# Performance work log

Measured on AMD Instinct MI355X. Metric: run time of the kernel, lower is better.

Reference implementation:

```python
import jax, jax.numpy as jnp
import numpy as np

EPS = 1e-06
BANDWIDTH = 0.1  # scipy minimize x0; frozen on first forward in the original


def _pairwise_sqdist(a, b):
    # a: [B, N, 3], b: [B, M, 3] -> [B, N, M] squared euclidean distances
    a2 = jnp.sum(a * a, axis=-1)  # [B, N]
    b2 = jnp.sum(b * b, axis=-1)  # [B, M]
    ab = jnp.einsum('bnd,bmd->bnm', a, b)  # [B, N, M]
    return jnp.maximum(a2[:, :, None] + b2[:, None, :] - 2.0 * ab, 0.0)


def _compute_density(points, bandwidth):
    # Gaussian KDE over all pairs (self included), normalized by N-1,
    # matching compute_density in the torch source.
    n = points.shape[1]
    sqd = _pairwise_sqdist(points, points)  # [B, N, N]
    kde = jnp.exp(-0.5 * sqd / (bandwidth * bandwidth))
    return jnp.sum(kde, axis=2) / (n - 1)  # [B, N]


def setup_inputs() -> dict:
    key = jax.random.key(0)
    k1, k2 = jax.random.split(key)
    predicted = jax.random.normal(k1, (8, 4096, 3), dtype=jnp.float32)
    ground_truth = jax.random.normal(k2, (8, 4096, 3), dtype=jnp.float32)
    return {
        'predicted': predicted,
        'ground_truth': ground_truth,
        'bandwidth_pred': jnp.float32(BANDWIDTH),
        'bandwidth_gt': jnp.float32(BANDWIDTH),
    }


def reference(predicted, ground_truth, bandwidth_pred, bandwidth_gt):
    # Chamfer distance: per-point squared distance to nearest neighbor in the
    # other cloud (standard ChamferDistance CUDA ext returns squared dists).
    sqd = _pairwise_sqdist(predicted, ground_truth)  # [B, N, M]
    dist_pred_to_gt = jnp.min(sqd, axis=2)  # [B, N]
    dist_gt_to_pred = jnp.min(sqd, axis=1)  # [B, M]

    density_pred = _compute_density(predicted, bandwidth_pred)  # [B, N]
    density_gt = _compute_density(ground_truth, bandwidth_gt)   # [B, M]

    loss_pred_to_gt = jnp.mean(dist_pred_to_gt / (density_pred + EPS))
    loss_gt_to_pred = jnp.mean(dist_gt_to_pred / (density_gt + EPS))
    return loss_pred_to_gt + loss_gt_to_pred
```

## Files before the change

kernel.cpp:

```cpp
#include <hip/hip_runtime.h>


#define NPTS 4096
#define NB   8
#define TS   128
#define TPB  256
#define BIGF 3.4e38f

__device__ __forceinline__ void unpack8(const float4* s4, int base,
                                        float (&X)[8], float (&Y)[8], float (&Z)[8])
{
    float4 A = s4[base+0], B = s4[base+1], C = s4[base+2];
    float4 D = s4[base+3], E = s4[base+4], F = s4[base+5];
    X[0]=A.x; Y[0]=A.y; Z[0]=A.z;  X[1]=A.w; Y[1]=B.x; Z[1]=B.y;
    X[2]=B.z; Y[2]=B.w; Z[2]=C.x;  X[3]=C.y; Y[3]=C.z; Z[3]=C.w;
    X[4]=D.x; Y[4]=D.y; Z[4]=D.z;  X[5]=D.w; Y[5]=E.x; Z[5]=E.y;
    X[6]=E.z; Y[6]=E.w; Z[6]=F.x;  X[7]=F.y; Y[7]=F.z; Z[7]=F.w;
}

__global__ __launch_bounds__(TPB) void dacl_pairs(
    const float* __restrict__ pred, const float* __restrict__ gt,
    const float* __restrict__ bwp,  const float* __restrict__ bwg,
    float* __restrict__ minP2G, float* __restrict__ minG2P,
    float* __restrict__ densP,  float* __restrict__ densG)
{
    __shared__ float4 sCol[1536];
    __shared__ float4 sRow[96];
    float* sRed = (float*)sCol;

    const int tid  = threadIdx.x;
    const int ty   = tid & 15;
    const int tx   = tid >> 4;
    const int wave = tid >> 6;
    const int lane = tid & 63;

    const int bid  = blockIdx.x;
    const int kind = bid % 6;
    const int rem  = bid / 6;
    const int b    = rem & 7;
    const int RT   = rem >> 3;

    const float* rowsrc; const float* colsrc; float scale;
    if (kind == 0)      { rowsrc = pred; colsrc = gt;   scale = 1.0f; }
    else if (kind == 1) { rowsrc = gt;   colsrc = pred; scale = 1.0f; }
    else if (kind < 4)  { rowsrc = pred; colsrc = pred;
                          const float bw = bwp[0];
                          scale = sqrtf(0.5f/(bw*bw*0.6931471805599453f)); }
    else                { rowsrc = gt;   colsrc = gt;
                          const float bw = bwg[0];
                          scale = sqrtf(0.5f/(bw*bw*0.6931471805599453f)); }

    const float4* rbase = (const float4*)(rowsrc + ((size_t)b*NPTS + RT*TS)*3);
    const float4* cbase = (const float4*)(colsrc + (size_t)b*NPTS*3);

    if (tid < 96) {
        float4 v = rbase[tid];
        v.x *= scale; v.y *= scale; v.z *= scale; v.w *= scale;
        sRow[tid] = v;
    }

    if (kind < 2) {
        float rx[8], ry[8], rz[8], rr[8], rmin[8];
        #pragma unroll
        for (int r = 0; r < 8; ++r) rmin[r] = BIGF;
        bool gotRows = false;

        for (int ph = 0; ph < 2; ++ph) {
            const float4* src = cbase + ph*1536;
            __syncthreads();
            #pragma unroll
            for (int i = 0; i < 6; ++i) sCol[tid + i*TPB] = src[tid + i*TPB];
            __syncthreads();
            if (!gotRows) {
                unpack8(sRow, ty*6, rx, ry, rz);
                #pragma unroll
                for (int r = 0; r < 8; ++r)
                    rr[r] = fmaf(rx[r],rx[r], fmaf(ry[r],ry[r], rz[r]*rz[r]));
                gotRows = true;
            }
            for (int t = 0; t < 16; ++t) {
                float cx[8], cy[8], cz[8];
                unpack8(sCol, t*96 + tx*6, cx, cy, cz);
                #pragma unroll
                for (int c = 0; c < 8; ++c) {
                    const float ax = -2.0f*cx[c], ay = -2.0f*cy[c], az = -2.0f*cz[c];
                    const float cc = fmaf(cx[c],cx[c], fmaf(cy[c],cy[c], cz[c]*cz[c]));
                    #pragma unroll
                    for (int r = 0; r < 8; ++r) {
                        float tv = fmaf(ax, rx[r], cc);
                        tv = fmaf(ay, ry[r], tv);
                        tv = fmaf(az, rz[r], tv);
                        rmin[r] = fminf(rmin[r], tv);
                    }
                }
            }
        }
        float v[8];
        #pragma unroll
        for (int r = 0; r < 8; ++r) {
            float m = fmaxf(rmin[r] + rr[r], 0.0f);
            m = fminf(m, __shfl_xor(m, 16, 64));
            m = fminf(m, __shfl_xor(m, 32, 64));
            v[r] = m;
        }
        __syncthreads();
        if (wave > 0 && lane < 16) {
            #pragma unroll
            for (int r = 0; r < 8; ++r) sRed[(wave-1)*128 + lane*8 + r] = v[r];
        }
        __syncthreads();
        if (wave == 0 && lane < 16) {
            float* out = (kind == 0 ? minP2G : minG2P) + b*NPTS + RT*TS + lane*8;
            #pragma unroll
            for (int r = 0; r < 8; ++r) {
                const int o = lane*8 + r;
                out[r] = fminf(fminf(v[r], sRed[o]),
                               fminf(sRed[128 + o], sRed[256 + o]));
            }
        }
    } else {
        const int h = kind & 1;
        float* D = (kind < 4 ? densP : densG) + h*(NB*NPTS);

        const float4* src = cbase + h*1536;
        #pragma unroll
        for (int i = 0; i < 6; ++i) {
            float4 x = src[tid + i*TPB];
            x.x *= scale; x.y *= scale; x.z *= scale; x.w *= scale;
            sCol[tid + i*TPB] = x;
        }
        __syncthreads();

        float rx[8], ry[8], rz[8], nrr[8], racc[8];
        unpack8(sRow, ty*6, rx, ry, rz);
        #pragma unroll
        for (int r = 0; r < 8; ++r) {
            nrr[r]  = -fmaf(rx[r],rx[r], fmaf(ry[r],ry[r], rz[r]*rz[r]));
            racc[r] = 0.0f;
        }

        for (int t = 0; t < 16; ++t) {
            float cx[8], cy[8], cz[8];
            unpack8(sCol, t*96 + tx*6, cx, cy, cz);
            #pragma unroll
            for (int c = 0; c < 8; ++c) {
                const float ax = 2.0f*cx[c], ay = 2.0f*cy[c], az = 2.0f*cz[c];
                const float ncc = fmaf(-cx[c],cx[c], fmaf(-cy[c],cy[c], -cz[c]*cz[c]));
                #pragma unroll
                for (int r = 0; r < 8; ++r) {
                    float e = fmaf(ax, rx[r], ncc);
                    e = fmaf(ay, ry[r], e);
                    e = fmaf(az, rz[r], e);
                    e = e + nrr[r];
                    racc[r] += __builtin_amdgcn_exp2f(e);
                }
            }
        }
        float v[8];
        #pragma unroll
        for (int r = 0; r < 8; ++r) {
            float s = racc[r];
            s += __shfl_xor(s, 16, 64);
            s += __shfl_xor(s, 32, 64);
            v[r] = s;
        }
        __syncthreads();
        if (wave > 0 && lane < 16) {
            #pragma unroll
            for (int r = 0; r < 8; ++r) sRed[(wave-1)*128 + lane*8 + r] = v[r];
        }
        __syncthreads();
        if (wave == 0 && lane < 16) {
            float* out = D + b*NPTS + RT*TS + lane*8;
            #pragma unroll
            for (int r = 0; r < 8; ++r) {
                const int o = lane*8 + r;
                out[r] = (v[r] + sRed[o]) + (sRed[128 + o] + sRed[256 + o]);
            }
        }
    }
}

__global__ __launch_bounds__(256) void dacl_combine(
    const float* __restrict__ minP2G, const float* __restrict__ minG2P,
    const float* __restrict__ densP, const float* __restrict__ densG,
    float* __restrict__ bsum)
{
    const int g   = blockIdx.x * 256 + threadIdx.x;
    const int dir = g >> 15;
    const int idx = g & 32767;
    const float m  = dir ? minG2P[idx] : minP2G[idx];
    const float dn = dir ? (densG[idx] + densG[idx + NB*NPTS])
                         : (densP[idx] + densP[idx + NB*NPTS]);
    float val = m / (dn * (1.0f/4095.0f) + 1e-6f) * (1.0f/32768.0f);

    #pragma unroll
    for (int off = 32; off; off >>= 1) val += __shfl_down(val, off);
    __shared__ float sm[4];
    const int lane = threadIdx.x & 63, wid = threadIdx.x >> 6;
    if (lane == 0) sm[wid] = val;
    __syncthreads();
    if (threadIdx.x == 0) bsum[blockIdx.x] = (sm[0] + sm[1]) + (sm[2] + sm[3]);
}

__global__ __launch_bounds__(256) void dacl_final(
    const float* __restrict__ bsum, float* __restrict__ out)
{
    float v = bsum[threadIdx.x];
    #pragma unroll
    for (int off = 32; off; off >>= 1) v += __shfl_down(v, off);
    __shared__ float sm[4];
    const int lane = threadIdx.x & 63, wid = threadIdx.x >> 6;
    if (lane == 0) sm[wid] = v;
    __syncthreads();
    if (threadIdx.x == 0) out[0] = (sm[0] + sm[1]) + (sm[2] + sm[3]);
}

extern "C" void kernel_launch(void* const* d_in, const int* in_sizes, int n_in,
                              void* d_out, int out_size, void* d_ws, size_t ws_size,
                              hipStream_t stream)
{
    const float* pred = (const float*)d_in[0];
    const float* gt   = (const float*)d_in[1];
    const float* bwp  = (const float*)d_in[2];
    const float* bwg  = (const float*)d_in[3];

    float* minP2G = (float*)d_ws;
    float* minG2P = minP2G + NB*NPTS;
    float* densP  = minG2P + NB*NPTS;
    float* densG  = densP + 2*NB*NPTS;
    float* bsum   = densG + 2*NB*NPTS;

    dacl_pairs<<<1536, TPB, 0, stream>>>(pred, gt, bwp, bwg,
                                         minP2G, minG2P, densP, densG);
    dacl_combine<<<(2*NB*NPTS)/256, 256, 0, stream>>>(minP2G, minG2P, densP, densG, bsum);
    dacl_final<<<1, 256, 0, stream>>>(bsum, (float*)d_out);
}
```

Before: 81.68 us.

## Compute pairwise dot products with bf16x3 split MFMA and exploit density symmetry

Adds a prep kernel that splits scaled coordinates into three bf16 parts and packs them into MFMA operand layouts. The pair kernel then computes the cross-term dot products with 16x16x32 bf16 MFMA instead of scalar FMAs. For the KDE it evaluates only the upper triangle of the symmetric kernel matrix and writes row and column partial sums separately. Chamfer minima are computed in both directions from one pass over the cross matrix. The goal is to move the inner products onto matrix cores and halve the exp work, at the cost of extra workspace traffic, a heavier combine step and some precision risk from the bf16 split.

Measured after the change: 127.0 us. 55.5% more time.

```diff
diff --git a/kernel.cpp b/kernel.cpp
--- a/kernel.cpp
+++ b/kernel.cpp
@@ -1,197 +1,296 @@
 #include <hip/hip_runtime.h>
 
 
+#define NB 8
 #define NPTS 4096
-#define NB   8
-#define TS   128
-#define TPB  256
+#define PTSTOT 32768
 #define BIGF 3.4e38f
-
-__device__ __forceinline__ void unpack8(const float4* s4, int base,
-                                        float (&X)[8], float (&Y)[8], float (&Z)[8])
-{
-    float4 A = s4[base+0], B = s4[base+1], C = s4[base+2];
-    float4 D = s4[base+3], E = s4[base+4], F = s4[base+5];
-    X[0]=A.x; Y[0]=A.y; Z[0]=A.z;  X[1]=A.w; Y[1]=B.x; Z[1]=B.y;
-    X[2]=B.z; Y[2]=B.w; Z[2]=C.x;  X[3]=C.y; Y[3]=C.z; Z[3]=C.w;
-    X[4]=D.x; Y[4]=D.y; Z[4]=D.z;  X[5]=D.w; Y[5]=E.x; Z[5]=E.y;
-    X[6]=E.z; Y[6]=E.w; Z[6]=F.x;  X[7]=F.y; Y[7]=F.z; Z[7]=F.w;
-}
-
-__global__ __launch_bounds__(TPB) void dacl_pairs(
+#define OFFD_BLKS 2176
+#define CROSS_BLKS 1024
+#define DIAG_BLKS 512
+#define TRISLOT 3968
+
+typedef __attribute__((ext_vector_type(8))) short bf16x8;
+typedef __attribute__((ext_vector_type(4))) float f32x4;
+
+__device__ __forceinline__ unsigned bf16rne(float x){
+    unsigned u = __float_as_uint(x);
+    return (u + 0x7FFFu + ((u>>16)&1u)) >> 16;
+}
+__device__ __forceinline__ void split1(float x, unsigned& h, unsigned& m, unsigned& l){
+    h = bf16rne(x);
+    float r1 = x - __uint_as_float(h<<16);
+    m = bf16rne(r1);
+    l = bf16rne(r1 - __uint_as_float(m<<16));
+}
+__device__ __forceinline__ void packA(uint4* a, int base,
+    unsigned hx,unsigned mx,unsigned lx, unsigned hy,unsigned my,unsigned ly,
+    unsigned hz,unsigned mz,unsigned lz)
+{
+    a[base]    = make_uint4(hx|(hx<<16), mx|(mx<<16), hx|(lx<<16), hy|(hy<<16));
+    a[base+16] = make_uint4(my|(my<<16), hy|(ly<<16), hz|(hz<<16), mz|(mz<<16));
+    a[base+32] = make_uint4(hz|(lz<<16), 0u, 0u, 0u);
+    a[base+48] = make_uint4(0u,0u,0u,0u);
+}
+__device__ __forceinline__ void packB(uint4* a, int base,
+    unsigned hx,unsigned mx,unsigned lx, unsigned hy,unsigned my,unsigned ly,
+    unsigned hz,unsigned mz,unsigned lz)
+{
+    a[base]    = make_uint4(hx|(mx<<16), hx|(mx<<16), lx|(hx<<16), hy|(my<<16));
+    a[base+16] = make_uint4(hy|(my<<16), ly|(hy<<16), hz|(mz<<16), hz|(mz<<16));
+    a[base+32] = make_uint4(lz|(hz<<16), 0u, 0u, 0u);
+    a[base+48] = make_uint4(0u,0u,0u,0u);
+}
+
+__global__ __launch_bounds__(256) void dacl_prep(
     const float* __restrict__ pred, const float* __restrict__ gt,
     const float* __restrict__ bwp,  const float* __restrict__ bwg,
-    float* __restrict__ minP2G, float* __restrict__ minG2P,
-    float* __restrict__ densP,  float* __restrict__ densG)
-{
-    __shared__ float4 sCol[1536];
-    __shared__ float4 sRow[96];
-    float* sRed = (float*)sCol;
-
+    uint4* __restrict__ Ac, uint4* __restrict__ Bc,
+    uint4* __restrict__ Ap, uint4* __restrict__ Bp,
+    uint4* __restrict__ Ag, uint4* __restrict__ Bg,
+    float* __restrict__ rrP, float* __restrict__ ccG,
+    float* __restrict__ ndP, float* __restrict__ ndG)
+{
+    const int gid  = blockIdx.x*256 + threadIdx.x;
+    const int cl   = gid >> 15;
+    const int pidx = gid & 32767;
+    const int base = ((pidx>>4)<<6) + (pidx & 15);
+    const float* s = (cl ? gt : pred) + (size_t)pidx*3;
+    const float x = s[0], y = s[1], z = s[2];
+    const float n2 = x*x + y*y + z*z;
+    const float bw = cl ? bwg[0] : bwp[0];
+    const float s2 = 0.5f / (bw*bw*0.6931471805599453f);
+    const float q  = sqrtf(2.0f*s2);
+
+    unsigned hx,mx,lx,hy,my,ly,hz,mz,lz;
+    if (cl == 0) {
+        split1(-2.f*x,hx,mx,lx); split1(-2.f*y,hy,my,ly); split1(-2.f*z,hz,mz,lz);
+        packA(Ac, base, hx,mx,lx,hy,my,ly,hz,mz,lz);
+        split1(q*x,hx,mx,lx); split1(q*y,hy,my,ly); split1(q*z,hz,mz,lz);
+        packA(Ap, base, hx,mx,lx,hy,my,ly,hz,mz,lz);
+        packB(Bp, base, hx,mx,lx,hy,my,ly,hz,mz,lz);
+        rrP[pidx] = n2; ndP[pidx] = -s2*n2;
+    } else {
+        split1(x,hx,mx,lx); split1(y,hy,my,ly); split1(z,hz,mz,lz);
+        packB(Bc, base, hx,mx,lx,hy,my,ly,hz,mz,lz);
+        split1(q*x,hx,mx,lx); split1(q*y,hy,my,ly); split1(q*z,hz,mz,lz);
+        packA(Ag, base, hx,mx,lx,hy,my,ly,hz,mz,lz);
+        packB(Bg, base, hx,mx,lx,hy,my,ly,hz,mz,lz);
+        ccG[pidx] = n2; ndG[pidx] = -s2*n2;
+    }
+}
+
+__global__ __launch_bounds__(256) void dacl_pairs(
+    const uint4* __restrict__ Ac, const uint4* __restrict__ Bc,
+    const uint4* __restrict__ Ap, const uint4* __restrict__ Bp,
+    const uint4* __restrict__ Ag, const uint4* __restrict__ Bg,
+    const float* __restrict__ rrP, const float* __restrict__ ccG,
+    const float* __restrict__ ndP, const float* __restrict__ ndG,
+    float* __restrict__ minP2Gp,
+    float* __restrict__ minG2Pp,
+    float* __restrict__ densRowP,
+    float* __restrict__ densCol)
+{
+    __shared__ float sRed[4][128];
     const int tid  = threadIdx.x;
-    const int ty   = tid & 15;
-    const int tx   = tid >> 4;
-    const int wave = tid >> 6;
     const int lane = tid & 63;
-
+    const int w    = tid >> 6;
+    const int lq   = lane >> 4;
+    const int lr   = lane & 15;
     const int bid  = blockIdx.x;
-    const int kind = bid % 6;
-    const int rem  = bid / 6;
-    const int b    = rem & 7;
-    const int RT   = rem >> 3;
-
-    const float* rowsrc; const float* colsrc; float scale;
-    if (kind == 0)      { rowsrc = pred; colsrc = gt;   scale = 1.0f; }
-    else if (kind == 1) { rowsrc = gt;   colsrc = pred; scale = 1.0f; }
-    else if (kind < 4)  { rowsrc = pred; colsrc = pred;
-                          const float bw = bwp[0];
-                          scale = sqrtf(0.5f/(bw*bw*0.6931471805599453f)); }
-    else                { rowsrc = gt;   colsrc = gt;
-                          const float bw = bwg[0];
-                          scale = sqrtf(0.5f/(bw*bw*0.6931471805599453f)); }
-
-    const float4* rbase = (const float4*)(rowsrc + ((size_t)b*NPTS + RT*TS)*3);
-    const float4* cbase = (const float4*)(colsrc + (size_t)b*NPTS*3);
-
-    if (tid < 96) {
-        float4 v = rbase[tid];
-        v.x *= scale; v.y *= scale; v.z *= scale; v.w *= scale;
-        sRow[tid] = v;
-    }
-
-    if (kind < 2) {
-        float rx[8], ry[8], rz[8], rr[8], rmin[8];
-        #pragma unroll
-        for (int r = 0; r < 8; ++r) rmin[r] = BIGF;
-        bool gotRows = false;
-
-        for (int ph = 0; ph < 2; ++ph) {
-            const float4* src = cbase + ph*1536;
-            __syncthreads();
-            #pragma unroll
-            for (int i = 0; i < 6; ++i) sCol[tid + i*TPB] = src[tid + i*TPB];
-            __syncthreads();
-            if (!gotRows) {
-                unpack8(sRow, ty*6, rx, ry, rz);
+    const f32x4 z4 = {0.f,0.f,0.f,0.f};
+
+    if (bid < OFFD_BLKS) {
+        const int clb = bid / 136;
+        int rem = bid - clb*136;
+        const int b = clb & 7, cl = clb >> 3;
+        int u = 0;
+        for (; u < 31; ++u) { int nch = (279 - 8*u) >> 5; if (rem < nch) break; rem -= nch; }
+        const int cj = rem;
+        const int J0 = 8*u + 8 + 32*cj;
+
+        const uint4* Aarr = cl ? Ag : Ap;
+        const uint4* Barr = cl ? Bg : Bp;
+        const float* nd   = cl ? ndG : ndP;
+        float* dCol = densCol + (size_t)clb * (TRISLOT*16);
+
+        bf16x8 af[8]; f32x4 ndr[8]; float racc[8][4];
+        #pragma unroll
+        for (int g = 0; g < 8; ++g) {
+            af[g]  = *((const bf16x8*)(Aarr + (size_t)((b*256 + u*8 + g)*64 + lane)));
+            ndr[g] = *((const f32x4*)(nd + b*4096 + u*128 + g*16 + lq*4));
+            #pragma unroll
+            for (int r = 0; r < 4; ++r) racc[g][r] = 0.f;
+        }
+
+        for (int t = 0; t < 8; ++t) {
+            const int J = J0 + w*8 + t;
+            if (J < 256) {
+                bf16x8 bfv = *((const bf16x8*)(Barr + (size_t)((b*256 + J)*64 + lane)));
+                const float ndcv = nd[b*4096 + J*16 + lr];
+                float ca = 0.f;
                 #pragma unroll
-                for (int r = 0; r < 8; ++r)
-                    rr[r] = fmaf(rx[r],rx[r], fmaf(ry[r],ry[r], rz[r]*rz[r]));
-                gotRows = true;
-            }
-            for (int t = 0; t < 16; ++t) {
-                float cx[8], cy[8], cz[8];
-                unpack8(sCol, t*96 + tx*6, cx, cy, cz);
-                #pragma unroll
-                for (int c = 0; c < 8; ++c) {
-                    const float ax = -2.0f*cx[c], ay = -2.0f*cy[c], az = -2.0f*cz[c];
-                    const float cc = fmaf(cx[c],cx[c], fmaf(cy[c],cy[c], cz[c]*cz[c]));
+                for (int g = 0; g < 8; ++g) {
+                    f32x4 acc = __builtin_amdgcn_mfma_f32_16x16x32_bf16(af[g], bfv, z4, 0,0,0);
                     #pragma unroll
-                    for (int r = 0; r < 8; ++r) {
-                        float tv = fmaf(ax, rx[r], cc);
-                        tv = fmaf(ay, ry[r], tv);
-                        tv = fmaf(az, rz[r], tv);
-                        rmin[r] = fminf(rmin[r], tv);
+                    for (int r = 0; r < 4; ++r) {
+                        float e = (acc[r] + ndr[g][r]) + ndcv;
+                        float k = __builtin_amdgcn_exp2f(e);
+                        racc[g][r] += k;
+                        ca += k;
                     }
                 }
-            }
-        }
-        float v[8];
-        #pragma unroll
-        for (int r = 0; r < 8; ++r) {
-            float m = fmaxf(rmin[r] + rr[r], 0.0f);
-            m = fminf(m, __shfl_xor(m, 16, 64));
-            m = fminf(m, __shfl_xor(m, 32, 64));
-            v[r] = m;
-        }
+                ca += __shfl_xor(ca, 16, 64);
+                ca += __shfl_xor(ca, 32, 64);
+                const int q8 = J >> 3, r8 = J & 7;
+                const int baseJ = 4*q8*(q8-1) + r8*q8;
+                if (lane < 16) dCol[(baseJ + u)*16 + lane] = ca;
+            }
+        }
+        #pragma unroll
+        for (int g = 0; g < 8; ++g)
+            #pragma unroll
+            for (int r = 0; r < 4; ++r) {
+                float v = racc[g][r];
+                v += __shfl_xor(v, 1, 64);
+                v += __shfl_xor(v, 2, 64);
+                v += __shfl_xor(v, 4, 64);
+                v += __shfl_xor(v, 8, 64);
+                if (lr == 0) sRed[w][g*16 + lq*4 + r] = v;
+            }
         __syncthreads();
-        if (wave > 0 && lane < 16) {
-            #pragma unroll
-            for (int r = 0; r < 8; ++r) sRed[(wave-1)*128 + lane*8 + r] = v[r];
-        }
+        if (tid < 128) {
+            float v = (sRed[0][tid] + sRed[1][tid]) + (sRed[2][tid] + sRed[3][tid]);
+            densRowP[(size_t)((cj+1)*2 + cl)*PTSTOT + b*4096 + u*128 + tid] = v;
+        }
+    } else if (bid < OFFD_BLKS + CROSS_BLKS) {
+        const int cb = bid - OFFD_BLKS;
+        const int b = cb >> 7, I = (cb >> 2) & 31, ph = cb & 3;
+
+        bf16x8 af[8]; f32x4 rr[8]; float rmin[8][4];
+        #pragma unroll
+        for (int g = 0; g < 8; ++g) {
+            af[g] = *((const bf16x8*)(Ac + (size_t)((b*256 + I*8 + g)*64 + lane)));
+            rr[g] = *((const f32x4*)(rrP + b*4096 + I*128 + g*16 + lq*4));
+            #pragma unroll
+            for (int r = 0; r < 4; ++r) rmin[g][r] = BIGF;
+        }
+
+        for (int t = 0; t < 16; ++t) {
+            const int J = ph*64 + w*16 + t;
+            bf16x8 bfv = *((const bf16x8*)(Bc + (size_t)((b*256 + J)*64 + lane)));
+            const float ccv = ccG[b*4096 + J*16 + lr];
+            float cm = BIGF;
+            #pragma unroll
+            for (int g = 0; g < 8; ++g) {
+                f32x4 acc = __builtin_amdgcn_mfma_f32_16x16x32_bf16(af[g], bfv, z4, 0,0,0);
+                #pragma unroll
+                for (int r = 0; r < 4; ++r) {
+                    rmin[g][r] = fminf(rmin[g][r], acc[r] + ccv);
+                    cm         = fminf(cm,         acc[r] + rr[g][r]);
+                }
+            }
+            cm = fminf(cm, __shfl_xor(cm, 16, 64));
+            cm = fminf(cm, __shfl_xor(cm, 32, 64));
+            if (lane < 16)
+                minG2Pp[(size_t)I*PTSTOT + b*4096 + J*16 + lane] = cm + ccv;
+        }
+        #pragma unroll
+        for (int g = 0; g < 8; ++g)
+            #pragma unroll
+            for (int r = 0; r < 4; ++r) {
+                float v = rmin[g][r] + rr[g][r];
+                v = fminf(v, __shfl_xor(v, 1, 64));
+                v = fminf(v, __shfl_xor(v, 2, 64));
+                v = fminf(v, __shfl_xor(v, 4, 64));
+                v = fminf(v, __shfl_xor(v, 8, 64));
+                if (lr == 0) sRed[w][g*16 + lq*4 + r] = v;
+            }
         __syncthreads();
-        if (wave == 0 && lane < 16) {
-            float* out = (kind == 0 ? minP2G : minG2P) + b*NPTS + RT*TS + lane*8;
-            #pragma unroll
-            for (int r = 0; r < 8; ++r) {
-                const int o = lane*8 + r;
-                out[r] = fminf(fminf(v[r], sRed[o]),
-                               fminf(sRed[128 + o], sRed[256 + o]));
-            }
+        if (tid < 128) {
+            float v = fminf(fminf(sRed[0][tid], sRed[1][tid]),
+                            fminf(sRed[2][tid], sRed[3][tid]));
+            minP2Gp[(size_t)ph*PTSTOT + b*4096 + I*128 + tid] = v;
         }
     } else {
-        const int h = kind & 1;
-        float* D = (kind < 4 ? densP : densG) + h*(NB*NPTS);
-
-        const float4* src = cbase + h*1536;
-        #pragma unroll
-        for (int i = 0; i < 6; ++i) {
-            float4 x = src[tid + i*TPB];
-            x.x *= scale; x.y *= scale; x.z *= scale; x.w *= scale;
-            sCol[tid + i*TPB] = x;
-        }
-        __syncthreads();
-
-        float rx[8], ry[8], rz[8], nrr[8], racc[8];
-        unpack8(sRow, ty*6, rx, ry, rz);
-        #pragma unroll
-        for (int r = 0; r < 8; ++r) {
-            nrr[r]  = -fmaf(rx[r],rx[r], fmaf(ry[r],ry[r], rz[r]*rz[r]));
-            racc[r] = 0.0f;
-        }
-
-        for (int t = 0; t < 16; ++t) {
-            float cx[8], cy[8], cz[8];
-            unpack8(sCol, t*96 + tx*6, cx, cy, cz);
-            #pragma unroll
-            for (int c = 0; c < 8; ++c) {
-                const float ax = 2.0f*cx[c], ay = 2.0f*cy[c], az = 2.0f*cz[c];
-                const float ncc = fmaf(-cx[c],cx[c], fmaf(-cy[c],cy[c], -cz[c]*cz[c]));
+        const int db = bid - (OFFD_BLKS + CROSS_BLKS);
+        const int b = db & 7, u = (db >> 3) & 31, cl = db >> 8;
+        const uint4* Aarr = cl ? Ag : Ap;
+        const uint4* Barr = cl ? Bg : Bp;
+        const float* nd   = cl ? ndG : ndP;
+
+        const int gA0 = w*2;
+        bf16x8 af[2]; f32x4 ndr[2]; float racc[2][4];
+        #pragma unroll
+        for (int i = 0; i < 2; ++i) {
+            const int g = gA0 + i;
+            af[i]  = *((const bf16x8*)(Aarr + (size_t)((b*256 + u*8 + g)*64 + lane)));
+            ndr[i] = *((const f32x4*)(nd + b*4096 + u*128 + g*16 + lq*4));
+            #pragma unroll
+            for (int r = 0; r < 4; ++r) racc[i][r] = 0.f;
+        }
+        for (int gB = 0; gB < 8; ++gB) {
+            bf16x8 bfv = *((const bf16x8*)(Barr + (size_t)((b*256 + u*8 + gB)*64 + lane)));
+            const float ndcv = nd[b*4096 + u*128 + gB*16 + lr];
+            #pragma unroll
+            for (int i = 0; i < 2; ++i) {
+                f32x4 acc = __builtin_amdgcn_mfma_f32_16x16x32_bf16(af[i], bfv, z4, 0,0,0);
                 #pragma unroll
-                for (int r = 0; r < 8; ++r) {
-                    float e = fmaf(ax, rx[r], ncc);
-                    e = fmaf(ay, ry[r], e);
-                    e = fmaf(az, rz[r], e);
-                    e = e + nrr[r];
-                    racc[r] += __builtin_amdgcn_exp2f(e);
+                for (int r = 0; r < 4; ++r) {
+                    float e = (acc[r] + ndr[i][r]) + ndcv;
+                    racc[i][r] += __builtin_amdgcn_exp2f(e);
                 }
             }
         }
-        float v[8];
-        #pragma unroll
-        for (int r = 0; r < 8; ++r) {
-            float s = racc[r];
-            s += __shfl_xor(s, 16, 64);
-            s += __shfl_xor(s, 32, 64);
-            v[r] = s;
-        }
-        __syncthreads();
-        if (wave > 0 && lane < 16) {
-            #pragma unroll
-            for (int r = 0; r < 8; ++r) sRed[(wave-1)*128 + lane*8 + r] = v[r];
-        }
-        __syncthreads();
-        if (wave == 0 && lane < 16) {
-            float* out = D + b*NPTS + RT*TS + lane*8;
-            #pragma unroll
-            for (int r = 0; r < 8; ++r) {
-                const int o = lane*8 + r;
-                out[r] = (v[r] + sRed[o]) + (sRed[128 + o] + sRed[256 + o]);
-            }
-        }
+        #pragma unroll
+        for (int i = 0; i < 2; ++i)
+            #pragma unroll
+            for (int r = 0; r < 4; ++r) {
+                float v = racc[i][r];
+                v += __shfl_xor(v, 1, 64);
+                v += __shfl_xor(v, 2, 64);
+                v += __shfl_xor(v, 4, 64);
+                v += __shfl_xor(v, 8, 64);
+                if (lr == 0)
+                    densRowP[(size_t)cl*PTSTOT + b*4096 + u*128 + (gA0+i)*16 + lq*4 + r] = v;
+            }
     }
 }
 
 __global__ __launch_bounds__(256) void dacl_combine(
-    const float* __restrict__ minP2G, const float* __restrict__ minG2P,
-    const float* __restrict__ densP, const float* __restrict__ densG,
+    const float* __restrict__ minP2Gp, const float* __restrict__ minG2Pp,
+    const float* __restrict__ densRowP, const float* __restrict__ densCol,
     float* __restrict__ bsum)
 {
-    const int g   = blockIdx.x * 256 + threadIdx.x;
+    const int g   = blockIdx.x*256 + threadIdx.x;
     const int dir = g >> 15;
     const int idx = g & 32767;
-    const float m  = dir ? minG2P[idx] : minP2G[idx];
-    const float dn = dir ? (densG[idx] + densG[idx + NB*NPTS])
-                         : (densP[idx] + densP[idx + NB*NPTS]);
+    const int b   = idx >> 12;
+    const int pt  = idx & 4095;
+    const int cl  = dir;
+
+    float m = BIGF;
+    if (dir == 0) {
+        #pragma unroll
+        for (int s = 0; s < 4; ++s) m = fminf(m, minP2Gp[(size_t)s*PTSTOT + idx]);
+    } else {
+        #pragma unroll
+        for (int s = 0; s < 32; ++s) m = fminf(m, minG2Pp[(size_t)s*PTSTOT + idx]);
+    }
+    m = fmaxf(m, 0.0f);
+
+    float dn = densRowP[(size_t)cl*PTSTOT + idx];
+    const int u = pt >> 7;
+    const int nch = (279 - 8*u) >> 5;
+    #pragma unroll
+    for (int k = 1; k <= 8; ++k)
+        if (k <= nch) dn += densRowP[(size_t)(k*2 + cl)*PTSTOT + idx];
+    const int T = pt >> 4;
+    const int q8 = T >> 3;
+    const int baseT = 4*q8*(q8-1) + (T&7)*q8;
+    const float* dC = densCol + (size_t)(cl*8 + b)*(TRISLOT*16) + (pt & 15);
+    for (int up = 0; up < q8; ++up) dn += dC[(baseT + up)*16];
+
     float val = m / (dn * (1.0f/4095.0f) + 1e-6f) * (1.0f/32768.0f);
 
     #pragma unroll
@@ -225,14 +324,28 @@
     const float* bwp  = (const float*)d_in[2];
     const float* bwg  = (const float*)d_in[3];
 
-    float* minP2G = (float*)d_ws;
-    float* minG2P = minP2G + NB*NPTS;
-    float* densP  = minG2P + NB*NPTS;
-    float* densG  = densP + 2*NB*NPTS;
-    float* bsum   = densG + 2*NB*NPTS;
-
-    dacl_pairs<<<1536, TPB, 0, stream>>>(pred, gt, bwp, bwg,
-                                         minP2G, minG2P, densP, densG);
-    dacl_combine<<<(2*NB*NPTS)/256, 256, 0, stream>>>(minP2G, minG2P, densP, densG, bsum);
+    uint4* Ac = (uint4*)d_ws;
+    uint4* Bc = Ac + 131072;
+    uint4* Ap = Bc + 131072;
+    uint4* Bp = Ap + 131072;
+    uint4* Ag = Bp + 131072;
+    uint4* Bg = Ag + 131072;
+    float* rrP = (float*)(Bg + 131072);
+    float* ccG = rrP + PTSTOT;
+    float* ndP = ccG + PTSTOT;
+    float* ndG = ndP + PTSTOT;
+    float* minP2Gp  = ndG + PTSTOT;
+    float* minG2Pp  = minP2Gp + 4*(size_t)PTSTOT;
+    float* densRowP = minG2Pp + 32*(size_t)PTSTOT;
+    float* densCol  = densRowP + 18*(size_t)PTSTOT;
+    float* bsum     = densCol + (size_t)16*TRISLOT*16;
+
+    dacl_prep<<<256, 256, 0, stream>>>(pred, gt, bwp, bwg,
+                                       Ac, Bc, Ap, Bp, Ag, Bg,
+                                       rrP, ccG, ndP, ndG);
+    dacl_pairs<<<OFFD_BLKS + CROSS_BLKS + DIAG_BLKS, 256, 0, stream>>>(
+        Ac, Bc, Ap, Bp, Ag, Bg, rrP, ccG, ndP, ndG,
+        minP2Gp, minG2Pp, densRowP, densCol);
+    dacl_combine<<<256, 256, 0, stream>>>(minP2Gp, minG2Pp, densRowP, densCol, bsum);
     dacl_final<<<1, 256, 0, stream>>>(bsum, (float*)d_out);
 }
```
